# Kernel optimization log

Hardware: AMD Instinct MI355X
Metric: run time of the kernel (lower is better)

The kernel has to match this reference:

```python
import jax, jax.numpy as jnp
import numpy as np

MIN_NORM = 1e-15
PROJ_EPS = 4e-3  # float32 boundary eps used by hgcn PoincareBall.proj
C = 1.0          # curvature for every layer
N, E, D = 10000, 320000, 256


def _norm(x):
    return jnp.maximum(jnp.linalg.norm(x, axis=-1, keepdims=True), MIN_NORM)


def artanh(x):
    return jnp.arctanh(jnp.clip(x, -1 + 1e-7, 1 - 1e-7))


def proj(x, c):
    norm = _norm(x)
    maxnorm = (1.0 - PROJ_EPS) / jnp.sqrt(c)
    return jnp.where(norm > maxnorm, x / norm * maxnorm, x)


def expmap0(u, c):
    sqrt_c = jnp.sqrt(c)
    u_norm = _norm(u)
    return jnp.tanh(sqrt_c * u_norm) * u / (sqrt_c * u_norm)


def logmap0(p, c):
    sqrt_c = jnp.sqrt(c)
    p_norm = _norm(p)
    return artanh(sqrt_c * p_norm) * p / (sqrt_c * p_norm)


def mobius_add(x, y, c):
    x2 = jnp.sum(x * x, -1, keepdims=True)
    y2 = jnp.sum(y * y, -1, keepdims=True)
    xy = jnp.sum(x * y, -1, keepdims=True)
    num = (1 + 2 * c * xy + c * y2) * x + (1 - c * x2) * y
    denom = 1 + 2 * c * xy + c * c * x2 * y2
    return num / jnp.maximum(denom, MIN_NORM)


def mobius_matvec(m, x, c):
    sqrt_c = jnp.sqrt(c)
    x_norm = _norm(x)
    mx = x @ m.T
    mx_norm = _norm(mx)
    res = jnp.tanh(mx_norm / x_norm * artanh(sqrt_c * x_norm)) * mx / (mx_norm * sqrt_c)
    zero_row = jnp.all(mx == 0, axis=-1, keepdims=True)
    return jnp.where(zero_row, jnp.zeros_like(res), res)


def hgc_layer(h, W, b, edge_weight, edge_src, edge_dst, c):
    # HypLinear (dropout=0, eval mode)
    res = proj(mobius_matvec(W, h, c), c)
    hyp_bias = proj(expmap0(b[None, :], c), c)
    h = proj(mobius_add(res, hyp_bias, c), c)
    # HypAgg: tangent-space neighborhood aggregation (spmm over edge list)
    xt = logmap0(h, c)                                  # [N, D]
    msgs = edge_weight[:, None] * xt[edge_src]          # [E, D] irregular gather
    agg = jax.ops.segment_sum(msgs, edge_dst, num_segments=N)
    h = proj(expmap0(agg, c), c)
    # HypAct: relu in tangent space, map back with c_out
    xt = jax.nn.relu(logmap0(h, c))
    return proj(expmap0(xt, c), c)


def setup_inputs() -> dict:
    key = jax.random.key(0)
    ks = jax.random.split(key, 8)
    x = jax.random.normal(ks[0], (N, D), dtype=jnp.float32)
    edge_src = jax.random.randint(ks[1], (E,), 0, N)
    edge_dst = jax.random.randint(ks[2], (E,), 0, N)
    # normalized-adjacency-like positive weights (~1/deg scale)
    edge_weight = jax.random.uniform(ks[3], (E,), dtype=jnp.float32) / 32.0
    s = 1.0 / np.sqrt(D)
    W1 = jax.random.normal(ks[4], (D, D), dtype=jnp.float32) * s
    b1 = jnp.zeros((D,), dtype=jnp.float32)
    W2 = jax.random.normal(ks[5], (D, D), dtype=jnp.float32) * s
    b2 = jnp.zeros((D,), dtype=jnp.float32)
    return {"x": x, "W1": W1, "b1": b1, "W2": W2, "b2": b2,
            "edge_weight": edge_weight, "edge_src": edge_src, "edge_dst": edge_dst}


def reference(x, W1, b1, W2, b2, edge_weight, edge_src, edge_dst):
    # old=True path: map Euclidean features onto the Poincare ball first
    h = proj(expmap0(x, C), C)
    h = hgc_layer(h, W1, b1, edge_weight, edge_src, edge_dst, C)
    h = hgc_layer(h, W2, b2, edge_weight, edge_src, edge_dst, C)
    return h
```

## Files before the change

### kernel.cpp

```cpp
#include <hip/hip_runtime.h>
#include <hip/hip_fp16.h>

#define DIM 256
#define MAXNORM 0.996f
#define MINN 1e-15f
#define CLIPV 0.9999999f

typedef __attribute__((ext_vector_type(8))) short bf16x8;
typedef __attribute__((ext_vector_type(4))) float f32x4;

__device__ __forceinline__ unsigned short f2bf(float f) {
    unsigned int u = __float_as_uint(f);
    u += 0x7fffu + ((u >> 16) & 1u);
    return (unsigned short)(u >> 16);
}
__device__ __forceinline__ float h2f(unsigned short h) {
    return __half2float(__ushort_as_half(h));
}
__device__ __forceinline__ unsigned short f2h(float f) {
    return __half_as_ushort(__float2half(f));
}
__device__ __forceinline__ float wsum(float v) {
    v += __shfl_xor(v, 32);
    v += __shfl_xor(v, 16);
    v += __shfl_xor(v, 8);
    v += __shfl_xor(v, 4);
    v += __shfl_xor(v, 2);
    v += __shfl_xor(v, 1);
    return v;
}
__device__ __forceinline__ float gsum16(float v) {
    v += __shfl_xor(v, 8);
    v += __shfl_xor(v, 4);
    v += __shfl_xor(v, 2);
    v += __shfl_xor(v, 1);
    return v;
}

__global__ void k_setup(const float* __restrict__ x, unsigned short* __restrict__ h_bf,
                        float* __restrict__ hnorm2, int nrows,
                        int* __restrict__ csr_off, int nOff,
                        const float* __restrict__ W1, const float* __restrict__ W2,
                        unsigned short* __restrict__ w_bf, int nPerW, int eB) {
    int bid = blockIdx.x;
    if (bid < eB) {
        int gid = bid * 256 + threadIdx.x;
        int row = gid >> 6, lane = gid & 63;
        if (row >= nrows) return;
        size_t base = (size_t)row * DIM + lane * 4;
        float4 v = *(const float4*)(x + base);
        float ss = wsum(v.x * v.x + v.y * v.y + v.z * v.z + v.w * v.w);
        float n = fmaxf(sqrtf(ss), MINN);
        float tn = tanhf(n);
        float hn = (tn > MAXNORM) ? MAXNORM : tn;
        float s = hn / n;
        ushort4 ob;
        ob.x = f2bf(v.x * s); ob.y = f2bf(v.y * s);
        ob.z = f2bf(v.z * s); ob.w = f2bf(v.w * s);
        *(ushort4*)(h_bf + base) = ob;
        if (lane == 0) hnorm2[row] = hn * hn;
    } else if (bid < eB + 64) {
        int i = (bid - eB) * 256 + threadIdx.x;
        int stride = 64 * 256;
        for (; i < nOff; i += stride) csr_off[i] = 0;
    } else {
        int i = (bid - eB - 64) * 256 + threadIdx.x;
        int stride = 128 * 256;
        for (; i < 2 * nPerW; i += stride)
            w_bf[i] = f2bf(i < nPerW ? W1[i] : W2[i - nPerW]);
    }
}

__global__ void k_hist(const int* __restrict__ dst, int* __restrict__ off, int nE, int nrows) {
    int e = blockIdx.x * blockDim.x + threadIdx.x;
    if (e >= nE) return;
    int d = dst[e];
    if (d >= 0 && d < nrows) atomicAdd(&off[d + 1], 1);
}

__global__ void k_scan(int* __restrict__ a, int* __restrict__ cursor, int n) {
    __shared__ int wsums[16];
    int t = threadIdx.x;
    int chunk = (n + 1023) / 1024;
    int lo = t * chunk, hi = min(lo + chunk, n);
    int sum = 0;
    for (int i = lo; i < hi; ++i) sum += a[i];
    int lane = t & 63, wid = t >> 6;
    int v = sum;
    for (int o = 1; o < 64; o <<= 1) {
        int u = __shfl_up(v, o);
        if (lane >= o) v += u;
    }
    if (lane == 63) wsums[wid] = v;
    __syncthreads();
    if (t == 0) {
        int c = 0;
        for (int i = 0; i < 16; ++i) { int x = wsums[i]; wsums[i] = c; c += x; }
    }
    __syncthreads();
    int excl = v - sum + wsums[wid];
    int c = excl;
    for (int i = lo; i < hi; ++i) {
        c += a[i];
        a[i] = c;
        if (i < n - 1) cursor[i] = c;
    }
}

__global__ void k_fill(const int* __restrict__ esrc, const int* __restrict__ edst,
                       const float* __restrict__ ew, int* __restrict__ cursor,
                       int2* __restrict__ csr_pack, int nE, int nrows) {
    int e = blockIdx.x * blockDim.x + threadIdx.x;
    if (e >= nE) return;
    int d = edst[e];
    if (d < 0 || d >= nrows) return;
    int pos = atomicAdd(&cursor[d], 1);
    csr_pack[pos] = make_int2(esrc[e], __float_as_int(ew[e]));
}

__global__ void __launch_bounds__(256) k_gemm_post(
                            const unsigned short* __restrict__ Abf,
                            const unsigned short* __restrict__ Wbf,
                            const float* __restrict__ hnorm2,
                            const float* __restrict__ bias,
                            unsigned short* __restrict__ XT, int M) {
    __shared__ float lds_sm[4][16];
    __shared__ float lds_sxy[4][16];
    int wave = threadIdx.x >> 6;
    int lane = threadIdx.x & 63;
    int r = lane & 15, oct = lane >> 4;
    int i0 = blockIdx.x * 16;
    int arow = i0 + r;
    bool av = arow < M;
    int jtbase = wave * 4;
    const unsigned short* ap = Abf + (size_t)(av ? arow : 0) * DIM + oct * 8;
    const unsigned short* wp = Wbf + (size_t)(jtbase * 16 + r) * DIM + oct * 8;
    const bf16x8 zf = {0, 0, 0, 0, 0, 0, 0, 0};
    f32x4 acc[4];
#pragma unroll
    for (int j = 0; j < 4; ++j) acc[j] = (f32x4){0.f, 0.f, 0.f, 0.f};
#pragma unroll
    for (int k0 = 0; k0 < 256; k0 += 32) {
        bf16x8 a = av ? *(const bf16x8*)(ap + k0) : zf;
#pragma unroll
        for (int j = 0; j < 4; ++j) {
            bf16x8 w = *(const bf16x8*)(wp + (size_t)j * 16 * DIM + k0);
            acc[j] = __builtin_amdgcn_mfma_f32_16x16x32_bf16(a, w, acc[j], 0, 0, 0);
        }
    }
    float bss = 0.f;
#pragma unroll
    for (int jt = 0; jt < 16; ++jt) {
        float b = bias[jt * 16 + r];
        bss = fmaf(b, b, bss);
    }
    bss = gsum16(bss);
    float bn = fmaxf(sqrtf(bss), MINN);
    float btn = tanhf(bn);
    float bhn = (btn > MAXNORM) ? MAXNORM : btn;
    float bscale = bhn / bn;
    float y2 = bhn * bhn;
    float bvw[4];
#pragma unroll
    for (int j = 0; j < 4; ++j) bvw[j] = bias[(jtbase + j) * 16 + r] * bscale;

#pragma unroll
    for (int q = 0; q < 4; ++q) {
        float sm = 0.f, sxy = 0.f;
#pragma unroll
        for (int j = 0; j < 4; ++j) {
            float m = acc[j][q];
            sm  = fmaf(m, m, sm);
            sxy = fmaf(m, bvw[j], sxy);
        }
        sm = gsum16(sm);
        sxy = gsum16(sxy);
        if (r == 0) {
            lds_sm[wave][oct * 4 + q] = sm;
            lds_sxy[wave][oct * 4 + q] = sxy;
        }
    }
    __syncthreads();
#pragma unroll
    for (int q = 0; q < 4; ++q) {
        int row16 = oct * 4 + q;
        int row = i0 + row16;
        float sm  = lds_sm[0][row16] + lds_sm[1][row16] + lds_sm[2][row16] + lds_sm[3][row16];
        float sxy = lds_sxy[0][row16] + lds_sxy[1][row16] + lds_sxy[2][row16] + lds_sxy[3][row16];
        if (row < M) {
            float sh = hnorm2[row];
            float xn = fmaxf(sqrtf(sh), MINN);
            float at = atanhf(fminf(xn, CLIPV));
            float mn = fmaxf(sqrtf(sm), MINN);
            float t = tanhf(mn / xn * at);
            float alpha = t / mn;
            float resn = t;
            if (t > MAXNORM) { alpha = MAXNORM / mn; resn = MAXNORM; }
            float x2 = resn * resn;
            float xy = alpha * sxy;
            float Aa = 1.f + 2.f * xy + y2;
            float Bb = 1.f - x2;
            float den = fmaxf(1.f + 2.f * xy + x2 * y2, MINN);
            float s_m = Aa * alpha / den;
            float s_b = Bb / den;
            float hn2 = (Aa * Aa * x2 + 2.f * Aa * Bb * xy + Bb * Bb * y2) / (den * den);
            float hn = fmaxf(sqrtf(fmaxf(hn2, 0.f)), MINN);
            if (hn > MAXNORM) { float f = MAXNORM / hn; s_m *= f; s_b *= f; hn = MAXNORM; }
            float lt = atanhf(fminf(hn, CLIPV)) / hn;
            s_m *= lt; s_b *= lt;
#pragma unroll
            for (int j = 0; j < 4; ++j)
                XT[(size_t)row * DIM + (jtbase + j) * 16 + r] =
                    f2h(fmaf(s_m, acc[j][q], s_b * bvw[j]));
        }
    }
}

__global__ void k_agg_finish(const unsigned short* __restrict__ XT, const int* __restrict__ off,
                             const int2* __restrict__ cpk,
                             float* __restrict__ OUT, unsigned short* __restrict__ OUT_bf,
                             float* __restrict__ hnorm2, int nrows) {
    int gid = blockIdx.x * blockDim.x + threadIdx.x;
    int row = gid >> 6, lane = gid & 63;
    if (row >= nrows) return;
    int p0 = off[row], p1 = off[row + 1];
    float a0 = 0.f, a1 = 0.f, a2 = 0.f, a3 = 0.f;
    int p = p0;
    for (; p + 7 < p1; p += 8) {
        ushort4 v[8];
        float w[8];
#pragma unroll
        for (int u = 0; u < 8; ++u) {
            int2 pk = cpk[p + u];
            w[u] = __int_as_float(pk.y);
            v[u] = *(const ushort4*)(XT + (size_t)pk.x * DIM + lane * 4);
        }
#pragma unroll
        for (int u = 0; u < 8; ++u) {
            a0 = fmaf(w[u], h2f(v[u].x), a0);
            a1 = fmaf(w[u], h2f(v[u].y), a1);
            a2 = fmaf(w[u], h2f(v[u].z), a2);
            a3 = fmaf(w[u], h2f(v[u].w), a3);
        }
    }
    for (; p < p1; ++p) {
        int2 pk = cpk[p];
        float w = __int_as_float(pk.y);
        ushort4 v = *(const ushort4*)(XT + (size_t)pk.x * DIM + lane * 4);
        a0 = fmaf(w, h2f(v.x), a0); a1 = fmaf(w, h2f(v.y), a1);
        a2 = fmaf(w, h2f(v.z), a2); a3 = fmaf(w, h2f(v.w), a3);
    }
    float ss = wsum(a0 * a0 + a1 * a1 + a2 * a2 + a3 * a3);
    float n = fmaxf(sqrtf(ss), MINN);
    float tn = tanhf(n);
    float hn = (tn > MAXNORM) ? MAXNORM : tn;
    float s1 = hn / n;
    float lt = atanhf(fminf(hn, CLIPV)) / fmaxf(hn, MINN);
    float s2 = lt * s1;
    float x0 = fmaxf(s2 * a0, 0.f), x1 = fmaxf(s2 * a1, 0.f);
    float x2 = fmaxf(s2 * a2, 0.f), x3 = fmaxf(s2 * a3, 0.f);
    float ss2 = wsum(x0 * x0 + x1 * x1 + x2 * x2 + x3 * x3);
    float n2 = fmaxf(sqrtf(ss2), MINN);
    float tn2 = tanhf(n2);
    float hn2c = (tn2 > MAXNORM) ? MAXNORM : tn2;
    float s3 = hn2c / n2;
    float o0 = s3 * x0, o1 = s3 * x1, o2 = s3 * x2, o3 = s3 * x3;
    size_t base = (size_t)row * DIM + lane * 4;
    if (OUT_bf) {
        ushort4 ob;
        ob.x = f2bf(o0); ob.y = f2bf(o1); ob.z = f2bf(o2); ob.w = f2bf(o3);
        *(ushort4*)(OUT_bf + base) = ob;
        if (lane == 0) hnorm2[row] = hn2c * hn2c;
    } else {
        *(float4*)(OUT + base) = make_float4(o0, o1, o2, o3);
    }
}

static inline size_t align256(size_t x) { return (x + 255) & ~(size_t)255; }

extern "C" void kernel_launch(void* const* d_in, const int* in_sizes, int n_in,
                              void* d_out, int out_size, void* d_ws, size_t ws_size,
                              hipStream_t stream) {
    const float* x  = (const float*)d_in[0];
    const float* W1 = (const float*)d_in[1];
    const float* b1 = (const float*)d_in[2];
    const float* W2 = (const float*)d_in[3];
    const float* b2 = (const float*)d_in[4];
    const float* ew = (const float*)d_in[5];
    const int* esrc = (const int*)d_in[6];
    const int* edst = (const int*)d_in[7];
    const int nE = in_sizes[5];
    const int M  = in_sizes[0] / DIM;

    size_t S = (size_t)M * DIM;
    char* base = (char*)d_ws;
    size_t o = 0;
    int2* csr_pack = (int2*)(base + o);          o = align256(o + (size_t)nE * 8);
    int* csr_off   = (int*)(base + o);           o = align256(o + (size_t)(M + 1) * 4);
    int* cursor    = (int*)(base + o);           o = align256(o + (size_t)M * 4);
    float* hnorm2  = (float*)(base + o);         o = align256(o + (size_t)(M + 64) * 4);
    unsigned short* xt   = (unsigned short*)(base + o);  o = align256(o + S * 2);
    unsigned short* h_bf = (unsigned short*)(base + o);  o = align256(o + S * 2);
    unsigned short* w_bf = (unsigned short*)(base + o);  o = align256(o + (size_t)2 * DIM * DIM * 2);

    int rowBlocks = (M + 3) / 4;
    int edgeBlocks = (nE + 255) / 256;

    k_setup<<<rowBlocks + 64 + 128, 256, 0, stream>>>(
        x, h_bf, hnorm2, M, csr_off, M + 1, W1, W2, w_bf, DIM * DIM, rowBlocks);

    k_hist<<<edgeBlocks, 256, 0, stream>>>(edst, csr_off, nE, M);
    k_scan<<<1, 1024, 0, stream>>>(csr_off, cursor, M + 1);
    k_fill<<<edgeBlocks, 256, 0, stream>>>(esrc, edst, ew, cursor, csr_pack, nE, M);

    for (int layer = 0; layer < 2; ++layer) {
        const float* b = (layer == 0) ? b1 : b2;
        const unsigned short* Wb = w_bf + (size_t)layer * DIM * DIM;
        k_gemm_post<<<(M + 15) / 16, 256, 0, stream>>>(h_bf, Wb, hnorm2, b, xt, M);
        k_agg_finish<<<rowBlocks, 256, 0, stream>>>(
            xt, csr_off, csr_pack,
            (layer == 0) ? (float*)nullptr : (float*)d_out,
            (layer == 0) ? h_bf : (unsigned short*)nullptr,
            hnorm2, M);
    }
}
```

Measured before the change: 233.5 us.

## Fuse whole pipeline into one cooperative persistent kernel with grid syncs

Replaces the chain of separate launches with a single cooperative kernel: setup, CSR histogram, scan, fill, and both layers' GEMM and aggregation stages. Stages are separated by grid-wide barriers on a fixed 512-block persistent grid. It also switches the scan to a two-level per-block plus block-sum prefix. The aim is to remove kernel launch gaps and inter-kernel drain. The cost is fewer blocks for the GEMM phase and the overhead of several grid.sync barriers. If the cooperative launch fails, it falls back to the old multi-kernel path.

```diff
diff --git a/kernel.cpp b/kernel.cpp
--- a/kernel.cpp
+++ b/kernel.cpp
@@ -1,10 +1,14 @@
 #include <hip/hip_runtime.h>
 #include <hip/hip_fp16.h>
+#include <hip/hip_cooperative_groups.h>
+
+namespace cg = cooperative_groups;
 
 #define DIM 256
 #define MAXNORM 0.996f
 #define MINN 1e-15f
 #define CLIPV 0.9999999f
+#define COOP_GRID 512
 
 typedef __attribute__((ext_vector_type(8))) short bf16x8;
 typedef __attribute__((ext_vector_type(4))) float f32x4;
@@ -35,6 +39,244 @@
     v += __shfl_xor(v, 2);
     v += __shfl_xor(v, 1);
     return v;
+}
+
+struct MegaArgs {
+    const float* x; const float* W1; const float* b1; const float* W2; const float* b2;
+    const float* ew; const int* esrc; const int* edst;
+    int nE, M;
+    int2* csr_pack; int* csr_off; int* cursor; int* blocksum;
+    float* hnorm2; unsigned short* xt; unsigned short* h_bf; unsigned short* w_bf;
+    float* OUT;
+};
+
+__global__ void __launch_bounds__(256, 2) k_mega(MegaArgs A) {
+    cg::grid_group grid = cg::this_grid();
+    __shared__ int   wtot[4];
+    __shared__ float lds_sm[4][16];
+    __shared__ float lds_sxy[4][16];
+
+    const int tid = threadIdx.x, bid = blockIdx.x;
+    const int G = gridDim.x;
+    const int gthread = bid * 256 + tid;
+    const int NT = G * 256;
+    const int lane = tid & 63;
+    const int wid_g = gthread >> 6;
+    const int nwaves = NT >> 6;
+    const int M = A.M;
+
+    for (int row = wid_g; row < M; row += nwaves) {
+        size_t base = (size_t)row * DIM + lane * 4;
+        float4 v = *(const float4*)(A.x + base);
+        float ss = wsum(v.x * v.x + v.y * v.y + v.z * v.z + v.w * v.w);
+        float n = fmaxf(sqrtf(ss), MINN);
+        float tn = tanhf(n);
+        float hn = (tn > MAXNORM) ? MAXNORM : tn;
+        float s = hn / n;
+        ushort4 ob;
+        ob.x = f2bf(v.x * s); ob.y = f2bf(v.y * s);
+        ob.z = f2bf(v.z * s); ob.w = f2bf(v.w * s);
+        *(ushort4*)(A.h_bf + base) = ob;
+        if (lane == 0) A.hnorm2[row] = hn * hn;
+    }
+    for (int i = gthread; i < 2 * DIM * DIM; i += NT)
+        A.w_bf[i] = f2bf(i < DIM * DIM ? A.W1[i] : A.W2[i - DIM * DIM]);
+    for (int i = gthread; i < M + 1; i += NT) A.csr_off[i] = 0;
+    grid.sync();
+
+    for (int e = gthread; e < A.nE; e += NT) {
+        int d = A.edst[e];
+        if (d >= 0 && d < M) atomicAdd(&A.csr_off[d + 1], 1);
+    }
+    grid.sync();
+
+    const int n = M + 1;
+    int myincl = 0;
+    {
+        int v = (gthread < n) ? A.csr_off[gthread] : 0;
+        for (int o = 1; o < 64; o <<= 1) {
+            int u = __shfl_up(v, o);
+            if (lane >= o) v += u;
+        }
+        int wid = tid >> 6;
+        if (lane == 63) wtot[wid] = v;
+        __syncthreads();
+        int pre = 0;
+        for (int w = 0; w < wid; ++w) pre += wtot[w];
+        myincl = v + pre;
+        if (tid == 255) A.blocksum[bid] = myincl;
+    }
+    grid.sync();
+
+    if (gthread < n) {
+        int pre = 0;
+        for (int b = 0; b < bid; ++b) pre += A.blocksum[b];
+        int fin = myincl + pre;
+        A.csr_off[gthread] = fin;
+        if (gthread < n - 1) A.cursor[gthread] = fin;
+    }
+    grid.sync();
+
+    for (int e = gthread; e < A.nE; e += NT) {
+        int d = A.edst[e];
+        if (d >= 0 && d < M) {
+            int pos = atomicAdd(&A.cursor[d], 1);
+            A.csr_pack[pos] = make_int2(A.esrc[e], __float_as_int(A.ew[e]));
+        }
+    }
+    grid.sync();
+
+    const int wave = tid >> 6;
+    const int r = lane & 15, oct = lane >> 4;
+    const int groups = (M + 15) / 16;
+    for (int layer = 0; layer < 2; ++layer) {
+        const float* bias = layer ? A.b2 : A.b1;
+        const unsigned short* Wb = A.w_bf + (size_t)layer * DIM * DIM;
+
+        for (int g = bid; g < groups; g += G) {
+            int i0 = g * 16;
+            int arow = i0 + r;
+            bool av = arow < M;
+            int jtbase = wave * 4;
+            const unsigned short* ap = A.h_bf + (size_t)(av ? arow : 0) * DIM + oct * 8;
+            const unsigned short* wp = Wb + (size_t)(jtbase * 16 + r) * DIM + oct * 8;
+            const bf16x8 zf = {0, 0, 0, 0, 0, 0, 0, 0};
+            f32x4 acc[4];
+#pragma unroll
+            for (int j = 0; j < 4; ++j) acc[j] = (f32x4){0.f, 0.f, 0.f, 0.f};
+#pragma unroll
+            for (int k0 = 0; k0 < 256; k0 += 32) {
+                bf16x8 a = av ? *(const bf16x8*)(ap + k0) : zf;
+#pragma unroll
+                for (int j = 0; j < 4; ++j) {
+                    bf16x8 w = *(const bf16x8*)(wp + (size_t)j * 16 * DIM + k0);
+                    acc[j] = __builtin_amdgcn_mfma_f32_16x16x32_bf16(a, w, acc[j], 0, 0, 0);
+                }
+            }
+            float bss = 0.f;
+#pragma unroll
+            for (int jt = 0; jt < 16; ++jt) {
+                float b = bias[jt * 16 + r];
+                bss = fmaf(b, b, bss);
+            }
+            bss = gsum16(bss);
+            float bn = fmaxf(sqrtf(bss), MINN);
+            float btn = tanhf(bn);
+            float bhn = (btn > MAXNORM) ? MAXNORM : btn;
+            float bscale = bhn / bn;
+            float y2 = bhn * bhn;
+            float bvw[4];
+#pragma unroll
+            for (int j = 0; j < 4; ++j) bvw[j] = bias[(jtbase + j) * 16 + r] * bscale;
+#pragma unroll
+            for (int q = 0; q < 4; ++q) {
+                float sm = 0.f, sxy = 0.f;
+#pragma unroll
+                for (int j = 0; j < 4; ++j) {
+                    float m = acc[j][q];
+                    sm  = fmaf(m, m, sm);
+                    sxy = fmaf(m, bvw[j], sxy);
+                }
+                sm = gsum16(sm);
+                sxy = gsum16(sxy);
+                if (r == 0) {
+                    lds_sm[wave][oct * 4 + q] = sm;
+                    lds_sxy[wave][oct * 4 + q] = sxy;
+                }
+            }
+            __syncthreads();
+#pragma unroll
+            for (int q = 0; q < 4; ++q) {
+                int row16 = oct * 4 + q;
+                int row = i0 + row16;
+                float sm  = lds_sm[0][row16] + lds_sm[1][row16] + lds_sm[2][row16] + lds_sm[3][row16];
+                float sxy = lds_sxy[0][row16] + lds_sxy[1][row16] + lds_sxy[2][row16] + lds_sxy[3][row16];
+                if (row < M) {
+                    float sh = A.hnorm2[row];
+                    float xn = fmaxf(sqrtf(sh), MINN);
+                    float at = atanhf(fminf(xn, CLIPV));
+                    float mn = fmaxf(sqrtf(sm), MINN);
+                    float t = tanhf(mn / xn * at);
+                    float alpha = t / mn;
+                    float resn = t;
+                    if (t > MAXNORM) { alpha = MAXNORM / mn; resn = MAXNORM; }
+                    float x2 = resn * resn;
+                    float xy = alpha * sxy;
+                    float Aa = 1.f + 2.f * xy + y2;
+                    float Bb = 1.f - x2;
+                    float den = fmaxf(1.f + 2.f * xy + x2 * y2, MINN);
+                    float s_m = Aa * alpha / den;
+                    float s_b = Bb / den;
+                    float hn2 = (Aa * Aa * x2 + 2.f * Aa * Bb * xy + Bb * Bb * y2) / (den * den);
+                    float hn = fmaxf(sqrtf(fmaxf(hn2, 0.f)), MINN);
+                    if (hn > MAXNORM) { float f = MAXNORM / hn; s_m *= f; s_b *= f; hn = MAXNORM; }
+                    float lt = atanhf(fminf(hn, CLIPV)) / hn;
+                    s_m *= lt; s_b *= lt;
+#pragma unroll
+                    for (int j = 0; j < 4; ++j)
+                        A.xt[(size_t)row * DIM + (jtbase + j) * 16 + r] =
+                            f2h(fmaf(s_m, acc[j][q], s_b * bvw[j]));
+                }
+            }
+            __syncthreads();
+        }
+        grid.sync();
+
+        for (int row = wid_g; row < M; row += nwaves) {
+            int p0 = A.csr_off[row], p1 = A.csr_off[row + 1];
+            float a0 = 0.f, a1 = 0.f, a2 = 0.f, a3 = 0.f;
+            int p = p0;
+            for (; p + 7 < p1; p += 8) {
+                ushort4 v[8];
+                float w[8];
+#pragma unroll
+                for (int u = 0; u < 8; ++u) {
+                    int2 pk = A.csr_pack[p + u];
+                    w[u] = __int_as_float(pk.y);
+                    v[u] = *(const ushort4*)(A.xt + (size_t)pk.x * DIM + lane * 4);
+                }
+#pragma unroll
+                for (int u = 0; u < 8; ++u) {
+                    a0 = fmaf(w[u], h2f(v[u].x), a0);
+                    a1 = fmaf(w[u], h2f(v[u].y), a1);
+                    a2 = fmaf(w[u], h2f(v[u].z), a2);
+                    a3 = fmaf(w[u], h2f(v[u].w), a3);
+                }
+            }
+            for (; p < p1; ++p) {
+                int2 pk = A.csr_pack[p];
+                float w = __int_as_float(pk.y);
+                ushort4 v = *(const ushort4*)(A.xt + (size_t)pk.x * DIM + lane * 4);
+                a0 = fmaf(w, h2f(v.x), a0); a1 = fmaf(w, h2f(v.y), a1);
+                a2 = fmaf(w, h2f(v.z), a2); a3 = fmaf(w, h2f(v.w), a3);
+            }
+            float ss = wsum(a0 * a0 + a1 * a1 + a2 * a2 + a3 * a3);
+            float nn = fmaxf(sqrtf(ss), MINN);
+            float tn = tanhf(nn);
+            float hn = (tn > MAXNORM) ? MAXNORM : tn;
+            float s1 = hn / nn;
+            float lt = atanhf(fminf(hn, CLIPV)) / fmaxf(hn, MINN);
+            float s2 = lt * s1;
+            float x0 = fmaxf(s2 * a0, 0.f), x1 = fmaxf(s2 * a1, 0.f);
+            float x2 = fmaxf(s2 * a2, 0.f), x3 = fmaxf(s2 * a3, 0.f);
+            float ss2 = wsum(x0 * x0 + x1 * x1 + x2 * x2 + x3 * x3);
+            float n2 = fmaxf(sqrtf(ss2), MINN);
+            float tn2 = tanhf(n2);
+            float hn2c = (tn2 > MAXNORM) ? MAXNORM : tn2;
+            float s3 = hn2c / n2;
+            float o0 = s3 * x0, o1 = s3 * x1, o2 = s3 * x2, o3 = s3 * x3;
+            size_t base = (size_t)row * DIM + lane * 4;
+            if (layer == 0) {
+                ushort4 ob;
+                ob.x = f2bf(o0); ob.y = f2bf(o1); ob.z = f2bf(o2); ob.w = f2bf(o3);
+                *(ushort4*)(A.h_bf + base) = ob;
+                if (lane == 0) A.hnorm2[row] = hn2c * hn2c;
+            } else {
+                *(float4*)(A.OUT + base) = make_float4(o0, o1, o2, o3);
+            }
+        }
+        grid.sync();
+    }
 }
 
 __global__ void k_setup(const float* __restrict__ x, unsigned short* __restrict__ h_bf,
@@ -95,7 +337,7 @@
     __syncthreads();
     if (t == 0) {
         int c = 0;
-        for (int i = 0; i < 16; ++i) { int x = wsums[i]; wsums[i] = c; c += x; }
+        for (int i = 0; i < 16; ++i) { int xq = wsums[i]; wsums[i] = c; c += xq; }
     }
     __syncthreads();
     int excl = v - sum + wsums[wid];
@@ -163,7 +405,6 @@
     float bvw[4];
 #pragma unroll
     for (int j = 0; j < 4; ++j) bvw[j] = bias[(jtbase + j) * 16 + r] * bscale;
-
 #pragma unroll
     for (int q = 0; q < 4; ++q) {
         float sm = 0.f, sxy = 0.f;
@@ -298,21 +539,33 @@
     int2* csr_pack = (int2*)(base + o);          o = align256(o + (size_t)nE * 8);
     int* csr_off   = (int*)(base + o);           o = align256(o + (size_t)(M + 1) * 4);
     int* cursor    = (int*)(base + o);           o = align256(o + (size_t)M * 4);
+    int* blocksum  = (int*)(base + o);           o = align256(o + (size_t)2048 * 4);
     float* hnorm2  = (float*)(base + o);         o = align256(o + (size_t)(M + 64) * 4);
     unsigned short* xt   = (unsigned short*)(base + o);  o = align256(o + S * 2);
     unsigned short* h_bf = (unsigned short*)(base + o);  o = align256(o + S * 2);
     unsigned short* w_bf = (unsigned short*)(base + o);  o = align256(o + (size_t)2 * DIM * DIM * 2);
 
+    MegaArgs A;
+    A.x = x; A.W1 = W1; A.b1 = b1; A.W2 = W2; A.b2 = b2;
+    A.ew = ew; A.esrc = esrc; A.edst = edst;
+    A.nE = nE; A.M = M;
+    A.csr_pack = csr_pack; A.csr_off = csr_off; A.cursor = cursor; A.blocksum = blocksum;
+    A.hnorm2 = hnorm2; A.xt = xt; A.h_bf = h_bf; A.w_bf = w_bf;
+    A.OUT = (float*)d_out;
+    void* args[] = { &A };
+    hipError_t err = hipLaunchCooperativeKernel((const void*)k_mega,
+                                                dim3(COOP_GRID), dim3(256),
+                                                args, 0, stream);
+    if (err == hipSuccess) return;
+    (void)hipGetLastError();
+
     int rowBlocks = (M + 3) / 4;
     int edgeBlocks = (nE + 255) / 256;
-
     k_setup<<<rowBlocks + 64 + 128, 256, 0, stream>>>(
         x, h_bf, hnorm2, M, csr_off, M + 1, W1, W2, w_bf, DIM * DIM, rowBlocks);
-
     k_hist<<<edgeBlocks, 256, 0, stream>>>(edst, csr_off, nE, M);
     k_scan<<<1, 1024, 0, stream>>>(csr_off, cursor, M + 1);
     k_fill<<<edgeBlocks, 256, 0, stream>>>(esrc, edst, ew, cursor, csr_pack, nE, M);
-
     for (int layer = 0; layer < 2; ++layer) {
         const float* b = (layer == 0) ? b1 : b2;
         const unsigned short* Wb = w_bf + (size_t)layer * DIM * DIM;
```

Result: slower. 774.0 us (+231.4%).
